# Performance work log

Hardware: AMD Instinct MI355X
Metric: run time of the kernel (lower is better)

Reference implementation:

```python
import jax, jax.numpy as jnp
import numpy as np

B, C, H, W = 4, 512, 64, 64
C8 = C // 8


def setup_inputs() -> dict:
    key = jax.random.key(0)
    ks = jax.random.split(key, 8)
    s = 0.02
    return {
        "x": jax.random.normal(ks[0], (B, C, H, W), dtype=jnp.float32),
        "wq": jax.random.normal(ks[1], (C8, C), dtype=jnp.float32) * s,
        "bq": jax.random.normal(ks[2], (C8,), dtype=jnp.float32) * s,
        "wk": jax.random.normal(ks[3], (C8, C), dtype=jnp.float32) * s,
        "bk": jax.random.normal(ks[4], (C8,), dtype=jnp.float32) * s,
        "wv": jax.random.normal(ks[5], (C, C), dtype=jnp.float32) * s,
        "bv": jax.random.normal(ks[6], (C,), dtype=jnp.float32) * s,
        "gamma": jax.random.normal(ks[7], (1,), dtype=jnp.float32),
    }


def reference(x, wq, bq, wk, bk, wv, bv, gamma):
    b, c, h, w = x.shape
    # 1x1 convs == per-pixel linear projections
    q = jnp.einsum('bchw,oc->bohw', x, wq) + bq[None, :, None, None]  # [B,C8,H,W]
    k = jnp.einsum('bchw,oc->bohw', x, wk) + bk[None, :, None, None]  # [B,C8,H,W]
    v = jnp.einsum('bchw,oc->bohw', x, wv) + bv[None, :, None, None]  # [B,C,H,W]
    qf = q.reshape(b, c // 8, h * w)  # [B,C8,HW]
    kf = k.reshape(b, c // 8, h * w)  # [B,C8,HW]
    # energy[b,i,j] = q_i . k_j, viewed as [B,H,W,H,W]; softmax over last dim
    energy = jnp.einsum('bci,bcj->bij', qf, kf).reshape(b, h, w, h, w)
    attn = jax.nn.softmax(energy, axis=-1)  # [B,H,W,H2,W2]
    # torch: out = bmm(value, permute(0,1,3,2,4).view(B,HW,HW))
    # rows index (h,h2) into value's spatial grid; cols index output (w,w2)
    out = jnp.einsum('bchk,bhwkv->bcwv', v, attn)  # [B,C,H,W]
    return gamma * out + x
```

## Files before the change

### kernel.cpp

```cpp
#include <hip/hip_runtime.h>
#include <hip/hip_bf16.h>


typedef __bf16 bf16_t;
typedef __bf16 bf16x8 __attribute__((ext_vector_type(8)));
typedef __bf16 bf16x4 __attribute__((ext_vector_type(4)));
typedef float f32x4 __attribute__((ext_vector_type(4)));

#define HW_ 4096
#define CIN 512
#define CQ 64

__device__ __forceinline__ void gload16(const void* g, void* l) {
  __builtin_amdgcn_global_load_lds((const __attribute__((address_space(1))) void*)g,
                                   (__attribute__((address_space(3))) void*)l, 16, 0, 0);
}

__global__ __launch_bounds__(256) void k_wcat(const float* __restrict__ wq,
                                              const float* __restrict__ wk,
                                              const float* __restrict__ wv,
                                              bf16_t* __restrict__ Wcat) {
  int idx = (blockIdx.x * 256 + threadIdx.x) * 4;
  int row = idx >> 9, c = idx & 511;
  const float* src;
  if (row < 64)       src = wq + row * 512 + c;
  else if (row < 128) src = wk + (row - 64) * 512 + c;
  else                src = wv + (row - 128) * 512 + c;
  float4 v = *(const float4*)src;
  bf16x4 o = { (bf16_t)v.x, (bf16_t)v.y, (bf16_t)v.z, (bf16_t)v.w };
  *(bf16x4*)&Wcat[idx] = o;
}

__global__ __launch_bounds__(256) void k_prep(const float* __restrict__ x, bf16_t* __restrict__ xT) {
  __shared__ float tile[64][65];
  const int b = blockIdx.z;
  const int p0 = blockIdx.x * 64, c0 = blockIdx.y * 64;
  const float* xb = x + (size_t)b * CIN * HW_;
  bf16_t* xTb = xT + (size_t)b * HW_ * CIN;
  const int tid = threadIdx.x;
  const int r = tid >> 4, q = tid & 15;
#pragma unroll
  for (int i = 0; i < 4; ++i) {
    int lr = r + 16 * i;
    float4 v = *(const float4*)&xb[(size_t)(c0 + lr) * HW_ + p0 + q * 4];
    tile[lr][q * 4 + 0] = v.x; tile[lr][q * 4 + 1] = v.y;
    tile[lr][q * 4 + 2] = v.z; tile[lr][q * 4 + 3] = v.w;
  }
  __syncthreads();
#pragma unroll
  for (int i = 0; i < 4; ++i) {
    int pr = r + 16 * i;
    bf16x4 o;
    o[0] = (bf16_t)tile[q * 4 + 0][pr];
    o[1] = (bf16_t)tile[q * 4 + 1][pr];
    o[2] = (bf16_t)tile[q * 4 + 2][pr];
    o[3] = (bf16_t)tile[q * 4 + 3][pr];
    *(bf16x4*)&xTb[(size_t)(p0 + pr) * CIN + c0 + q * 4] = o;
  }
}

__global__ __launch_bounds__(256) void k_projqk(const bf16_t* __restrict__ Wcat,
                                                const bf16_t* __restrict__ xT,
                                                const float* __restrict__ bq,
                                                const float* __restrict__ bk,
                                                bf16_t* __restrict__ qfT,
                                                bf16_t* __restrict__ kfT) {
  __shared__ bf16_t As[128][64];
  __shared__ bf16_t Bs[128][64];
  const int b = blockIdx.z;
  const int n0 = blockIdx.x * 128;
  const char* Wb = (const char*)Wcat;
  const char* Xb = (const char*)(xT + (size_t)b * HW_ * CIN);
  const int tid = threadIdx.x, wv_ = tid >> 6, lane = tid & 63;
  const int wm = wv_ >> 1, wn = wv_ & 1;
  const int g = lane >> 4, cc = lane & 15;
  f32x4 acc[4][4]{};
  for (int ks = 0; ks < 512; ks += 64) {
    if (ks) __syncthreads();
#pragma unroll
    for (int i = 0; i < 4; ++i) {
      int ch = wv_ * 4 + i;
      int rr = ch * 8 + (lane >> 3);
      int sl = (lane & 7) ^ (rr & 7);
      gload16(Wb + (size_t)rr * 1024 + ks * 2 + sl * 16, (char*)As + ch * 1024);
      gload16(Xb + (size_t)(n0 + rr) * 1024 + ks * 2 + sl * 16, (char*)Bs + ch * 1024);
    }
    __syncthreads();
#pragma unroll
    for (int k2 = 0; k2 < 2; ++k2) {
      bf16x8 a[4], bb[4];
#pragma unroll
      for (int f = 0; f < 4; ++f)
        a[f] = *(const bf16x8*)((char*)As + (wm * 64 + f * 16 + cc) * 128 + (((k2 * 4 + g) ^ (cc & 7)) * 16));
#pragma unroll
      for (int f = 0; f < 4; ++f)
        bb[f] = *(const bf16x8*)((char*)Bs + (wn * 64 + f * 16 + cc) * 128 + (((k2 * 4 + g) ^ (cc & 7)) * 16));
#pragma unroll
      for (int fm = 0; fm < 4; ++fm)
#pragma unroll
        for (int fn = 0; fn < 4; ++fn)
          acc[fm][fn] = __builtin_amdgcn_mfma_f32_16x16x32_bf16(a[fm], bb[fn], acc[fm][fn], 0, 0, 0);
    }
  }
  bf16_t* qb = qfT + (size_t)b * HW_ * CQ;
  bf16_t* kb = kfT + (size_t)b * HW_ * CQ;
#pragma unroll
  for (int fm = 0; fm < 4; ++fm) {
#pragma unroll
    for (int j = 0; j < 4; ++j) {
      int m = wm * 64 + fm * 16 + g * 4 + j;
      float bias = (m < 64) ? bq[m] : bk[m - 64];
#pragma unroll
      for (int fn = 0; fn < 4; ++fn) {
        int n = n0 + wn * 64 + fn * 16 + cc;
        float val = acc[fm][fn][j] + bias;
        if (m < 64) qb[(size_t)n * CQ + m] = (bf16_t)val;
        else        kb[(size_t)n * CQ + (m - 64)] = (bf16_t)val;
      }
    }
  }
}

__global__ __launch_bounds__(256) void k_projv(const bf16_t* __restrict__ Wcat,
                                               const bf16_t* __restrict__ xT,
                                               const float* __restrict__ bv,
                                               bf16_t* __restrict__ Vp2) {
  __shared__ bf16_t As[128][64];
  __shared__ bf16_t Bs[128][64];
  const int lin = blockIdx.x + blockIdx.y * 32 + blockIdx.z * 128;
  const int orig = (lin & 7) * 64 + (lin >> 3);
  const int bx = orig & 31, by = (orig >> 5) & 3, b = orig >> 7;
  const int n0 = bx * 128, m0 = by * 128;
  const char* Wb = (const char*)Wcat;
  const char* Xb = (const char*)(xT + (size_t)b * HW_ * CIN);
  const int tid = threadIdx.x, wv_ = tid >> 6, lane = tid & 63;
  const int wm = wv_ >> 1, wn = wv_ & 1;
  const int g = lane >> 4, cc = lane & 15;
  f32x4 acc[4][4]{};
  for (int ks = 0; ks < 512; ks += 64) {
    if (ks) __syncthreads();
#pragma unroll
    for (int i = 0; i < 4; ++i) {
      int ch = wv_ * 4 + i;
      int rr = ch * 8 + (lane >> 3);
      int sl = (lane & 7) ^ (rr & 7);
      int pix = (rr & 63) * 64 + (bx * 2) + (rr >> 6);
      gload16(Wb + (size_t)(128 + m0 + rr) * 1024 + ks * 2 + sl * 16, (char*)As + ch * 1024);
      gload16(Xb + (size_t)pix * 1024 + ks * 2 + sl * 16, (char*)Bs + ch * 1024);
    }
    __syncthreads();
#pragma unroll
    for (int k2 = 0; k2 < 2; ++k2) {
      bf16x8 a[4], bb[4];
#pragma unroll
      for (int f = 0; f < 4; ++f)
        a[f] = *(const bf16x8*)((char*)As + (wm * 64 + f * 16 + cc) * 128 + (((k2 * 4 + g) ^ (cc & 7)) * 16));
#pragma unroll
      for (int f = 0; f < 4; ++f)
        bb[f] = *(const bf16x8*)((char*)Bs + (wn * 64 + f * 16 + cc) * 128 + (((k2 * 4 + g) ^ (cc & 7)) * 16));
#pragma unroll
      for (int fm = 0; fm < 4; ++fm)
#pragma unroll
        for (int fn = 0; fn < 4; ++fn)
          acc[fm][fn] = __builtin_amdgcn_mfma_f32_16x16x32_bf16(a[fm], bb[fn], acc[fm][fn], 0, 0, 0);
    }
  }
  bf16_t* Vb = Vp2 + (size_t)b * CIN * HW_;
#pragma unroll
  for (int fm = 0; fm < 4; ++fm) {
#pragma unroll
    for (int j = 0; j < 4; ++j) {
      int m = m0 + wm * 64 + fm * 16 + g * 4 + j;
      float bias = bv[m];
#pragma unroll
      for (int fn = 0; fn < 4; ++fn) {
        int n = n0 + wn * 64 + fn * 16 + cc;
        Vb[(size_t)m * HW_ + n] = (bf16_t)(acc[fm][fn][j] + bias);
      }
    }
  }
}

__global__ __launch_bounds__(256) void k_energy(const bf16_t* __restrict__ qfT,
                                                const bf16_t* __restrict__ kfT,
                                                bf16_t* __restrict__ Pt, int zbase) {
  __shared__ bf16_t Qs[8192];
  __shared__ bf16_t Ks[2][4096];
  const int lin = blockIdx.x + blockIdx.y * 32 + blockIdx.z * 512;
  const int total = 512 * gridDim.z, chunk = total >> 3;
  const int orig = (lin & 7) * chunk + (lin >> 3);
  const int bx = orig & 31, by = (orig >> 5) & 15, bz = orig >> 9;
  const int b = zbase + bz;
  const int w0 = bx * 2, ky0 = by * 4;
  const char* qb = (const char*)(qfT + (size_t)b * HW_ * CQ);
  const char* kb = (const char*)(kfT + (size_t)b * HW_ * CQ);
  bf16_t* Ptb = Pt + (size_t)bz * 16777216;
  const int tid = threadIdx.x, wv_ = tid >> 6, lane = tid & 63;
  const int g = lane >> 4, cc = lane & 15;

#pragma unroll
  for (int i = 0; i < 4; ++i) {
    int ch = wv_ * 4 + i;
    int rr = ch * 8 + (lane >> 3);
    int sl = (lane & 7) ^ (rr & 7);
    int pix = (rr & 63) * 64 + w0 + (rr >> 6);
    gload16(qb + (size_t)pix * 128 + sl * 16, (char*)Qs + ch * 1024);
  }
#pragma unroll
  for (int i = 0; i < 2; ++i) {
    int ch = wv_ * 2 + i;
    int rr = ch * 8 + (lane >> 3);
    int sl = (lane & 7) ^ (rr & 7);
    gload16(kb + (size_t)(ky0 * 64 + rr) * 128 + sl * 16, (char*)Ks[0] + ch * 1024);
  }
  asm volatile("s_waitcnt vmcnt(0)" ::: "memory");
  __builtin_amdgcn_s_barrier();

  bf16x8 qf[2][2];
#pragma unroll
  for (int fm = 0; fm < 2; ++fm)
#pragma unroll
    for (int k2 = 0; k2 < 2; ++k2)
      qf[fm][k2] = *(const bf16x8*)((char*)Qs + (wv_ * 32 + fm * 16 + cc) * 128 +
                                    (((k2 * 4 + g) ^ (cc & 7)) * 16));

  const int w = w0 + (wv_ >> 1);
  for (int kq = 0; kq < 4; ++kq) {
    const int cur = kq & 1;
    if (kq < 3) {
      const int nxt = cur ^ 1;
#pragma unroll
      for (int i = 0; i < 2; ++i) {
        int ch = wv_ * 2 + i;
        int rr = ch * 8 + (lane >> 3);
        int sl = (lane & 7) ^ (rr & 7);
        gload16(kb + (size_t)((ky0 + kq + 1) * 64 + rr) * 128 + sl * 16, (char*)Ks[nxt] + ch * 1024);
      }
      asm volatile("s_waitcnt vmcnt(2)" ::: "memory");
    } else {
      asm volatile("s_waitcnt vmcnt(0)" ::: "memory");
    }
    __builtin_amdgcn_s_barrier();

    f32x4 acc[2][4]{};
#pragma unroll
    for (int k2 = 0; k2 < 2; ++k2) {
      bf16x8 kf[4];
#pragma unroll
      for (int f = 0; f < 4; ++f)
        kf[f] = *(const bf16x8*)((char*)Ks[cur] + (f * 16 + cc) * 128 + (((k2 * 4 + g) ^ (cc & 7)) * 16));
#pragma unroll
      for (int fm = 0; fm < 2; ++fm)
#pragma unroll
        for (int fn = 0; fn < 4; ++fn)
          acc[fm][fn] = __builtin_amdgcn_mfma_f32_16x16x32_bf16(qf[fm][k2], kf[fn], acc[fm][fn], 0, 0, 0);
    }
#pragma unroll
    for (int fm = 0; fm < 2; ++fm) {
      float e[4][4], invj[4];
#pragma unroll
      for (int j = 0; j < 4; ++j) {
        float mx = fmaxf(fmaxf(acc[fm][0][j], acc[fm][1][j]), fmaxf(acc[fm][2][j], acc[fm][3][j]));
#pragma unroll
        for (int d = 1; d < 16; d <<= 1) mx = fmaxf(mx, __shfl_xor(mx, d, 64));
        float s = 0.f;
#pragma unroll
        for (int fn = 0; fn < 4; ++fn) { e[fn][j] = __expf(acc[fm][fn][j] - mx); s += e[fn][j]; }
#pragma unroll
        for (int d = 1; d < 16; d <<= 1) s += __shfl_xor(s, d, 64);
        invj[j] = __builtin_amdgcn_rcpf(s);
      }
      int h0 = (wv_ & 1) * 32 + fm * 16 + g * 4;
#pragma unroll
      for (int fn = 0; fn < 4; ++fn) {
        int v = fn * 16 + cc;
        bf16x4 pk = { (bf16_t)(e[fn][0] * invj[0]), (bf16_t)(e[fn][1] * invj[1]),
                      (bf16_t)(e[fn][2] * invj[2]), (bf16_t)(e[fn][3] * invj[3]) };
        *(bf16x4*)&Ptb[(((size_t)w * 64 + (ky0 + kq)) * 64 + v) * 64 + h0] = pk;
      }
    }
    asm volatile("s_waitcnt lgkmcnt(0)" ::: "memory");
    __builtin_amdgcn_s_barrier();
  }
}

#define KSTEP_S(s, cur, nxt) do {                                                            \
    _Pragma("unroll")                                                                        \
    for (int r = 0; r < 4; ++r)                                                              \
      gload16(aSb[r] + (size_t)((s) + 1) * 128, Ls + (nxt) * 49152 + (r * 8 + wv_) * 1024);  \
    _Pragma("unroll")                                                                        \
    for (int r = 0; r < 2; ++r)                                                              \
      gload16(bSb[r] + (size_t)((s) + 1) * 8192,                                             \
              Ls + (nxt) * 49152 + 32768 + (r * 8 + wv_) * 1024);                            \
    asm volatile("s_waitcnt vmcnt(6)" ::: "memory");                                         \
    __builtin_amdgcn_s_barrier();                                                            \
    COMPUTE(cur);                                                                            \
  } while (0)

#define COMPUTE(cur) do {                                                                    \
    const char* base_ = Ls + (cur) * 49152;                                                  \
    _Pragma("unroll")                                                                        \
    for (int k2 = 0; k2 < 2; ++k2) {                                                         \
      bf16x8 a[4], bb[4];                                                                    \
      _Pragma("unroll")                                                                      \
      for (int fm = 0; fm < 4; ++fm) a[fm] = *(const bf16x8*)(base_ + aoff[k2][fm]);         \
      _Pragma("unroll")                                                                      \
      for (int fn = 0; fn < 4; ++fn) bb[fn] = *(const bf16x8*)(base_ + boff[k2][fn]);        \
      _Pragma("unroll")                                                                      \
      for (int fm = 0; fm < 4; ++fm)                                                         \
        _Pragma("unroll")                                                                    \
        for (int fn = 0; fn < 4; ++fn)                                                       \
          acc[fm][fn] = __builtin_amdgcn_mfma_f32_16x16x32_bf16(a[fm], bb[fn], acc[fm][fn], 0, 0, 0); \
    }                                                                                        \
  } while (0)

__global__ __launch_bounds__(512) void k_out(const bf16_t* __restrict__ Vp2,
                                             const bf16_t* __restrict__ Pt,
                                             const float* __restrict__ x,
                                             const float* __restrict__ gamma,
                                             float* __restrict__ outp, int zbase) {
  __shared__ char Ls[147456];
  const int lin = blockIdx.x + (blockIdx.y << 1) + (blockIdx.z << 6);
  const int nwg8 = (gridDim.z == 4) ? 32 : 8;
  const int rsw = (lin & 7) * nwg8 + (lin >> 3);
  const int c0 = (rsw & 1) * 256;
  const int w0 = ((rsw >> 1) & 31) * 2;
  const int bz = (gridDim.z == 4) ? (rsw >> 6) : 0;
  const int b = zbase + bz;
  const char* Vb = (const char*)(Vp2 + (size_t)b * CIN * HW_);
  const char* Pb = (const char*)(Pt + (size_t)bz * 16777216);
  const int tid = threadIdx.x, wv_ = tid >> 6, lane = tid & 63;
  const int wm = wv_ >> 1, wn = wv_ & 1;
  const int g = lane >> 4, cc = lane & 15;

  const char* aSb[4]; const char* bSb[2];
#pragma unroll
  for (int r = 0; r < 4; ++r) {
    int L = (r * 8 + wv_) * 64 + lane;
    int arow = L >> 3, asl = (L & 7) ^ (arow & 7);
    aSb[r] = Vb + (size_t)(c0 + arow) * 8192 + asl * 16;
  }
#pragma unroll
  for (int r = 0; r < 2; ++r) {
    int L = (r * 8 + wv_) * 64 + lane;
    int ws = L >> 9, e = L & 511, v = e >> 3, bsl = (e & 7) ^ (v & 7);
    bSb[r] = Pb + (size_t)(w0 + ws) * 524288 + v * 128 + bsl * 16;
  }
  int aoff[2][4], boff[2][4];
#pragma unroll
  for (int k2 = 0; k2 < 2; ++k2) {
#pragma unroll
    for (int fm = 0; fm < 4; ++fm)
      aoff[k2][fm] = (wm * 64 + fm * 16 + cc) * 128 + (((k2 * 4 + g) ^ (cc & 7)) * 16);
#pragma unroll
    for (int fn = 0; fn < 4; ++fn)
      boff[k2][fn] = 32768 + wn * 8192 + (fn * 16 + cc) * 128 + (((k2 * 4 + g) ^ (cc & 7)) * 16);
  }

  f32x4 acc[4][4]{};
#pragma unroll
  for (int r = 0; r < 4; ++r) gload16(aSb[r], Ls + (r * 8 + wv_) * 1024);
#pragma unroll
  for (int r = 0; r < 2; ++r) gload16(bSb[r], Ls + 32768 + (r * 8 + wv_) * 1024);

  int s = 0;
#pragma unroll 1
  for (int t = 0; t < 21; ++t) {
    KSTEP_S(s, 0, 1);
    KSTEP_S(s + 1, 1, 2);
    KSTEP_S(s + 2, 2, 0);
    s += 3;
  }
  asm volatile("s_waitcnt vmcnt(0)" ::: "memory");
  __builtin_amdgcn_s_barrier();
  COMPUTE(0);

  const float gmm = gamma[0];
  const float* xb = x + (size_t)b * CIN * HW_;
  float* ob = outp + (size_t)b * CIN * HW_;
  const int w = w0 + wn;
#pragma unroll
  for (int fm = 0; fm < 4; ++fm) {
#pragma unroll
    for (int jj = 0; jj < 4; ++jj) {
      int c = c0 + wm * 64 + fm * 16 + g * 4 + jj;
#pragma unroll
      for (int fn = 0; fn < 4; ++fn) {
        int n = w * 64 + fn * 16 + cc;
        size_t idx = (size_t)c * HW_ + n;
        ob[idx] = gmm * acc[fm][fn][jj] + xb[idx];
      }
    }
  }
}

extern "C" void kernel_launch(void* const* d_in, const int* in_sizes, int n_in,
                              void* d_out, int out_size, void* d_ws, size_t ws_size,
                              hipStream_t stream) {
  const float* x  = (const float*)d_in[0];
  const float* wq = (const float*)d_in[1];
  const float* bq = (const float*)d_in[2];
  const float* wk = (const float*)d_in[3];
  const float* bk = (const float*)d_in[4];
  const float* wv = (const float*)d_in[5];
  const float* bv = (const float*)d_in[6];
  const float* gamma = (const float*)d_in[7];
  float* outp = (float*)d_out;
  char* ws = (char*)d_ws;
  size_t off = 0;
  bf16_t* xT   = (bf16_t*)(ws + off); off += (size_t)4 * HW_ * CIN * 2;
  bf16_t* Wcat = (bf16_t*)(ws + off); off += (size_t)640 * CIN * 2;
  bf16_t* qfT  = (bf16_t*)(ws + off); off += (size_t)4 * HW_ * CQ * 2;
  bf16_t* kfT  = (bf16_t*)(ws + off); off += (size_t)4 * HW_ * CQ * 2;
  bf16_t* Vp2  = (bf16_t*)(ws + off); off += (size_t)4 * CIN * HW_ * 2;
  bf16_t* Pt   = (bf16_t*)(ws + off);
  const size_t pbytes = (size_t)HW_ * HW_ * 2;
  const bool full = (ws_size >= off + 4 * pbytes);

  k_wcat<<<dim3(320), dim3(256), 0, stream>>>(wq, wk, wv, Wcat);
  k_prep<<<dim3(64, 8, 4), dim3(256), 0, stream>>>(x, xT);
  k_projqk<<<dim3(32, 1, 4), dim3(256), 0, stream>>>(Wcat, xT, bq, bk, qfT, kfT);
  k_projv<<<dim3(32, 4, 4), dim3(256), 0, stream>>>(Wcat, xT, bv, Vp2);
  if (full) {
    k_energy<<<dim3(32, 16, 4), dim3(256), 0, stream>>>(qfT, kfT, Pt, 0);
    k_out<<<dim3(2, 32, 4), dim3(512), 0, stream>>>(Vp2, Pt, x, gamma, outp, 0);
  } else {
    for (int b = 0; b < 4; ++b) {
      k_energy<<<dim3(32, 16, 1), dim3(256), 0, stream>>>(qfT, kfT, Pt, b);
      k_out<<<dim3(2, 32, 1), dim3(512), 0, stream>>>(Vp2, Pt, x, gamma, outp, b);
    }
  }
}
```

Measured before the change: 170.7 us.

## Fuse Q/K/V projections into one GEMM kernel with permuted pixel ordering

Merges the separate QK and V projection kernels into a single 640-row GEMM launch with a swizzled block order. Q and K are now stored in the permuted (w,h) pixel order that the value projection already used, so the energy kernel loads its Q tile contiguously and walks K with strided per-row pointers. This removes one launch and the tail underfill of the small 128-block QK launch, at the cost of branchy epilogue stores and strided K loads in the energy kernel.

```diff
diff --git a/kernel.cpp b/kernel.cpp
--- a/kernel.cpp
+++ b/kernel.cpp
@@ -59,77 +59,19 @@
   }
 }
 
-__global__ __launch_bounds__(256) void k_projqk(const bf16_t* __restrict__ Wcat,
-                                                const bf16_t* __restrict__ xT,
-                                                const float* __restrict__ bq,
-                                                const float* __restrict__ bk,
-                                                bf16_t* __restrict__ qfT,
-                                                bf16_t* __restrict__ kfT) {
+__global__ __launch_bounds__(256) void k_proj(const bf16_t* __restrict__ Wcat,
+                                              const bf16_t* __restrict__ xT,
+                                              const float* __restrict__ bq,
+                                              const float* __restrict__ bk,
+                                              const float* __restrict__ bv,
+                                              bf16_t* __restrict__ qfT2,
+                                              bf16_t* __restrict__ kfT2,
+                                              bf16_t* __restrict__ Vp2) {
   __shared__ bf16_t As[128][64];
   __shared__ bf16_t Bs[128][64];
-  const int b = blockIdx.z;
-  const int n0 = blockIdx.x * 128;
-  const char* Wb = (const char*)Wcat;
-  const char* Xb = (const char*)(xT + (size_t)b * HW_ * CIN);
-  const int tid = threadIdx.x, wv_ = tid >> 6, lane = tid & 63;
-  const int wm = wv_ >> 1, wn = wv_ & 1;
-  const int g = lane >> 4, cc = lane & 15;
-  f32x4 acc[4][4]{};
-  for (int ks = 0; ks < 512; ks += 64) {
-    if (ks) __syncthreads();
-#pragma unroll
-    for (int i = 0; i < 4; ++i) {
-      int ch = wv_ * 4 + i;
-      int rr = ch * 8 + (lane >> 3);
-      int sl = (lane & 7) ^ (rr & 7);
-      gload16(Wb + (size_t)rr * 1024 + ks * 2 + sl * 16, (char*)As + ch * 1024);
-      gload16(Xb + (size_t)(n0 + rr) * 1024 + ks * 2 + sl * 16, (char*)Bs + ch * 1024);
-    }
-    __syncthreads();
-#pragma unroll
-    for (int k2 = 0; k2 < 2; ++k2) {
-      bf16x8 a[4], bb[4];
-#pragma unroll
-      for (int f = 0; f < 4; ++f)
-        a[f] = *(const bf16x8*)((char*)As + (wm * 64 + f * 16 + cc) * 128 + (((k2 * 4 + g) ^ (cc & 7)) * 16));
-#pragma unroll
-      for (int f = 0; f < 4; ++f)
-        bb[f] = *(const bf16x8*)((char*)Bs + (wn * 64 + f * 16 + cc) * 128 + (((k2 * 4 + g) ^ (cc & 7)) * 16));
-#pragma unroll
-      for (int fm = 0; fm < 4; ++fm)
-#pragma unroll
-        for (int fn = 0; fn < 4; ++fn)
-          acc[fm][fn] = __builtin_amdgcn_mfma_f32_16x16x32_bf16(a[fm], bb[fn], acc[fm][fn], 0, 0, 0);
-    }
-  }
-  bf16_t* qb = qfT + (size_t)b * HW_ * CQ;
-  bf16_t* kb = kfT + (size_t)b * HW_ * CQ;
-#pragma unroll
-  for (int fm = 0; fm < 4; ++fm) {
-#pragma unroll
-    for (int j = 0; j < 4; ++j) {
-      int m = wm * 64 + fm * 16 + g * 4 + j;
-      float bias = (m < 64) ? bq[m] : bk[m - 64];
-#pragma unroll
-      for (int fn = 0; fn < 4; ++fn) {
-        int n = n0 + wn * 64 + fn * 16 + cc;
-        float val = acc[fm][fn][j] + bias;
-        if (m < 64) qb[(size_t)n * CQ + m] = (bf16_t)val;
-        else        kb[(size_t)n * CQ + (m - 64)] = (bf16_t)val;
-      }
-    }
-  }
-}
-
-__global__ __launch_bounds__(256) void k_projv(const bf16_t* __restrict__ Wcat,
-                                               const bf16_t* __restrict__ xT,
-                                               const float* __restrict__ bv,
-                                               bf16_t* __restrict__ Vp2) {
-  __shared__ bf16_t As[128][64];
-  __shared__ bf16_t Bs[128][64];
-  const int lin = blockIdx.x + blockIdx.y * 32 + blockIdx.z * 128;
-  const int orig = (lin & 7) * 64 + (lin >> 3);
-  const int bx = orig & 31, by = (orig >> 5) & 3, b = orig >> 7;
+  const int lin = blockIdx.x + blockIdx.y * 32 + blockIdx.z * 160;
+  const int orig = (lin & 7) * 80 + (lin >> 3);
+  const int by = orig % 5, bx = (orig / 5) & 31, b = orig / 160;
   const int n0 = bx * 128, m0 = by * 128;
   const char* Wb = (const char*)Wcat;
   const char* Xb = (const char*)(xT + (size_t)b * HW_ * CIN);
@@ -145,7 +87,7 @@
       int rr = ch * 8 + (lane >> 3);
       int sl = (lane & 7) ^ (rr & 7);
       int pix = (rr & 63) * 64 + (bx * 2) + (rr >> 6);
-      gload16(Wb + (size_t)(128 + m0 + rr) * 1024 + ks * 2 + sl * 16, (char*)As + ch * 1024);
+      gload16(Wb + (size_t)(m0 + rr) * 1024 + ks * 2 + sl * 16, (char*)As + ch * 1024);
       gload16(Xb + (size_t)pix * 1024 + ks * 2 + sl * 16, (char*)Bs + ch * 1024);
     }
     __syncthreads();
@@ -165,24 +107,29 @@
           acc[fm][fn] = __builtin_amdgcn_mfma_f32_16x16x32_bf16(a[fm], bb[fn], acc[fm][fn], 0, 0, 0);
     }
   }
+  bf16_t* qb = qfT2 + (size_t)b * HW_ * CQ;
+  bf16_t* kb = kfT2 + (size_t)b * HW_ * CQ;
   bf16_t* Vb = Vp2 + (size_t)b * CIN * HW_;
 #pragma unroll
   for (int fm = 0; fm < 4; ++fm) {
 #pragma unroll
     for (int j = 0; j < 4; ++j) {
       int m = m0 + wm * 64 + fm * 16 + g * 4 + j;
-      float bias = bv[m];
+      float bias = (m < 64) ? bq[m] : (m < 128) ? bk[m - 64] : bv[m - 128];
 #pragma unroll
       for (int fn = 0; fn < 4; ++fn) {
         int n = n0 + wn * 64 + fn * 16 + cc;
-        Vb[(size_t)m * HW_ + n] = (bf16_t)(acc[fm][fn][j] + bias);
-      }
-    }
-  }
-}
-
-__global__ __launch_bounds__(256) void k_energy(const bf16_t* __restrict__ qfT,
-                                                const bf16_t* __restrict__ kfT,
+        float val = acc[fm][fn][j] + bias;
+        if (m < 64)       qb[(size_t)n * CQ + m] = (bf16_t)val;
+        else if (m < 128) kb[(size_t)n * CQ + (m - 64)] = (bf16_t)val;
+        else              Vb[(size_t)(m - 128) * HW_ + n] = (bf16_t)val;
+      }
+    }
+  }
+}
+
+__global__ __launch_bounds__(256) void k_energy(const bf16_t* __restrict__ qfT2,
+                                                const bf16_t* __restrict__ kfT2,
                                                 bf16_t* __restrict__ Pt, int zbase) {
   __shared__ bf16_t Qs[8192];
   __shared__ bf16_t Ks[2][4096];
@@ -192,8 +139,8 @@
   const int bx = orig & 31, by = (orig >> 5) & 15, bz = orig >> 9;
   const int b = zbase + bz;
   const int w0 = bx * 2, ky0 = by * 4;
-  const char* qb = (const char*)(qfT + (size_t)b * HW_ * CQ);
-  const char* kb = (const char*)(kfT + (size_t)b * HW_ * CQ);
+  const char* qb = (const char*)(qfT2 + (size_t)b * HW_ * CQ);
+  const char* kb = (const char*)(kfT2 + (size_t)b * HW_ * CQ);
   bf16_t* Ptb = Pt + (size_t)bz * 16777216;
   const int tid = threadIdx.x, wv_ = tid >> 6, lane = tid & 63;
   const int g = lane >> 4, cc = lane & 15;
@@ -203,15 +150,16 @@
     int ch = wv_ * 4 + i;
     int rr = ch * 8 + (lane >> 3);
     int sl = (lane & 7) ^ (rr & 7);
-    int pix = (rr & 63) * 64 + w0 + (rr >> 6);
-    gload16(qb + (size_t)pix * 128 + sl * 16, (char*)Qs + ch * 1024);
-  }
+    gload16(qb + (size_t)(w0 * 64 + rr) * 128 + sl * 16, (char*)Qs + ch * 1024);
+  }
+  const char* kSb[2];
 #pragma unroll
   for (int i = 0; i < 2; ++i) {
     int ch = wv_ * 2 + i;
     int rr = ch * 8 + (lane >> 3);
     int sl = (lane & 7) ^ (rr & 7);
-    gload16(kb + (size_t)(ky0 * 64 + rr) * 128 + sl * 16, (char*)Ks[0] + ch * 1024);
+    kSb[i] = kb + (size_t)rr * 8192 + ky0 * 128 + sl * 16;
+    gload16(kSb[i], (char*)Ks[0] + ch * 1024);
   }
   asm volatile("s_waitcnt vmcnt(0)" ::: "memory");
   __builtin_amdgcn_s_barrier();
@@ -232,9 +180,7 @@
 #pragma unroll
       for (int i = 0; i < 2; ++i) {
         int ch = wv_ * 2 + i;
-        int rr = ch * 8 + (lane >> 3);
-        int sl = (lane & 7) ^ (rr & 7);
-        gload16(kb + (size_t)((ky0 + kq + 1) * 64 + rr) * 128 + sl * 16, (char*)Ks[nxt] + ch * 1024);
+        gload16(kSb[i] + (kq + 1) * 128, (char*)Ks[nxt] + ch * 1024);
       }
       asm volatile("s_waitcnt vmcnt(2)" ::: "memory");
     } else {
@@ -410,8 +356,8 @@
   size_t off = 0;
   bf16_t* xT   = (bf16_t*)(ws + off); off += (size_t)4 * HW_ * CIN * 2;
   bf16_t* Wcat = (bf16_t*)(ws + off); off += (size_t)640 * CIN * 2;
-  bf16_t* qfT  = (bf16_t*)(ws + off); off += (size_t)4 * HW_ * CQ * 2;
-  bf16_t* kfT  = (bf16_t*)(ws + off); off += (size_t)4 * HW_ * CQ * 2;
+  bf16_t* qfT2 = (bf16_t*)(ws + off); off += (size_t)4 * HW_ * CQ * 2;
+  bf16_t* kfT2 = (bf16_t*)(ws + off); off += (size_t)4 * HW_ * CQ * 2;
   bf16_t* Vp2  = (bf16_t*)(ws + off); off += (size_t)4 * CIN * HW_ * 2;
   bf16_t* Pt   = (bf16_t*)(ws + off);
   const size_t pbytes = (size_t)HW_ * HW_ * 2;
@@ -419,14 +365,13 @@
 
   k_wcat<<<dim3(320), dim3(256), 0, stream>>>(wq, wk, wv, Wcat);
   k_prep<<<dim3(64, 8, 4), dim3(256), 0, stream>>>(x, xT);
-  k_projqk<<<dim3(32, 1, 4), dim3(256), 0, stream>>>(Wcat, xT, bq, bk, qfT, kfT);
-  k_projv<<<dim3(32, 4, 4), dim3(256), 0, stream>>>(Wcat, xT, bv, Vp2);
+  k_proj<<<dim3(32, 5, 4), dim3(256), 0, stream>>>(Wcat, xT, bq, bk, bv, qfT2, kfT2, Vp2);
   if (full) {
-    k_energy<<<dim3(32, 16, 4), dim3(256), 0, stream>>>(qfT, kfT, Pt, 0);
+    k_energy<<<dim3(32, 16, 4), dim3(256), 0, stream>>>(qfT2, kfT2, Pt, 0);
     k_out<<<dim3(2, 32, 4), dim3(512), 0, stream>>>(Vp2, Pt, x, gamma, outp, 0);
   } else {
     for (int b = 0; b < 4; ++b) {
-      k_energy<<<dim3(32, 16, 1), dim3(256), 0, stream>>>(qfT, kfT, Pt, b);
+      k_energy<<<dim3(32, 16, 1), dim3(256), 0, stream>>>(qfT2, kfT2, Pt, b);
       k_out<<<dim3(2, 32, 1), dim3(512), 0, stream>>>(Vp2, Pt, x, gamma, outp, b);
     }
   }
```

Result: faster. 157.7 us (-7.6%).
